# Optimization experiments

Measured on AMD Instinct MI355X. Metric: run time of the kernel, lower is better.

## Reference

```python
import jax, jax.numpy as jnp
import numpy as np

NUM_CLASSES = 10
LAMBDA_UNCERTAINTY = 0.5
IGNORE_INDEX = 10
B, H, W = 8, 512, 512


def setup_inputs() -> dict:
    key = jax.random.key(0)
    k1, k2 = jax.random.split(key)
    logits = jax.random.normal(k1, (B, NUM_CLASSES, H, W), dtype=jnp.float32)
    targets = jax.random.randint(k2, (B, H, W), 0, 11)  # includes ignore_index=10
    return {"logits": logits, "targets": targets}


def reference(logits, targets):
    C = NUM_CLASSES
    f32 = logits.dtype

    # entropy of the predicted distribution (torch adds 1e-8 inside log)
    probs = jax.nn.softmax(logits, axis=1)                      # [B,C,H,W]
    log_probs = jnp.log(probs + 1e-8)
    entropy = -jnp.sum(probs * log_probs, axis=1)               # [B,H,W]

    valid = targets != IGNORE_INDEX                             # [B,H,W] bool
    valid_f = valid.astype(f32)
    n_valid = jnp.sum(valid_f)                                  # scalar

    # single-pass scatter-mean replacing the per-class python loop
    t_clip = jnp.clip(targets, 0, C - 1)
    t_flat = t_clip.reshape(-1)
    v_flat = valid_f.reshape(-1)
    counts = jax.ops.segment_sum(v_flat, t_flat, num_segments=C)                    # n_c per class
    ent_sum = jax.ops.segment_sum(entropy.reshape(-1) * v_flat, t_flat, num_segments=C)

    has_samples = (counts > 0) & (n_valid > 0)
    w_base = jnp.where(has_samples, (n_valid - counts) / jnp.maximum(n_valid, 1.0), 0.0)
    entropy_mean = jnp.where(counts > 0, ent_sum / jnp.maximum(counts, 1.0), 0.0)
    w_combined = w_base * (1.0 + LAMBDA_UNCERTAINTY * entropy_mean)                 # [C]

    weight_map = w_combined[t_clip] * valid_f                   # [B,H,W]

    # per-pixel cross entropy, zeroed at ignore_index (torch F.cross_entropy semantics)
    log_sm = jax.nn.log_softmax(logits, axis=1)                 # [B,C,H,W]
    ce = -jnp.take_along_axis(log_sm, t_clip[:, None], axis=1)[:, 0]  # [B,H,W]
    ce = ce * valid_f

    return jnp.sum(ce * weight_map) / (n_valid + 1e-6)
```

## Files before the change

### kernel.cpp

```cpp
#include <hip/hip_runtime.h>

#define NCLS 10
#define IGN 10
#define HW_ (512 * 512)
#define BATCH 8
#define NPIX (BATCH * HW_)
#define THREADS 256
#define PIXPERTHREAD 4
#define NBLOCKS (NPIX / (THREADS * PIXPERTHREAD))
#define STAT_STRIDE 16
#define LAMBDA_UNC 0.5f

__global__ void awce_zero_stats(float* __restrict__ stats) {
    int i = threadIdx.x;
    if (i < 30 * STAT_STRIDE) stats[i] = 0.0f;
}

template <bool ATOMIC>
__global__ __launch_bounds__(THREADS) void awce_main(
    const float* __restrict__ logits,
    const int* __restrict__ targets,
    float* __restrict__ outbuf)
{
    const int gtid = blockIdx.x * THREADS + threadIdx.x;
    const int p0 = gtid * PIXPERTHREAD;
    const int b = p0 >> 18;
    const int hw = p0 & (HW_ - 1);
    const float* base = logits + (size_t)b * (NCLS * (size_t)HW_) + hw;

    float x[NCLS][4];
#pragma unroll
    for (int c = 0; c < NCLS; ++c) {
        float4 v = *reinterpret_cast<const float4*>(base + (size_t)c * HW_);
        x[c][0] = v.x; x[c][1] = v.y; x[c][2] = v.z; x[c][3] = v.w;
    }
    int4 t4 = *reinterpret_cast<const int4*>(targets + p0);
    int t[4] = {t4.x, t4.y, t4.z, t4.w};

    float cnt[NCLS], es[NCLS], cs[NCLS];
#pragma unroll
    for (int c = 0; c < NCLS; ++c) { cnt[c] = 0.f; es[c] = 0.f; cs[c] = 0.f; }

#pragma unroll
    for (int j = 0; j < PIXPERTHREAD; ++j) {
        const int tj = t[j];
        const bool valid = (tj != IGN);
        const int tc = valid ? tj : (NCLS - 1);

        float m = x[0][j];
#pragma unroll
        for (int c = 1; c < NCLS; ++c) m = fmaxf(m, x[c][j]);

        float s = 0.f, dot = 0.f, xt = 0.f;
#pragma unroll
        for (int c = 0; c < NCLS; ++c) {
            const float xc = x[c][j];
            const float e = __expf(xc - m);
            s += e;
            dot = fmaf(e, xc, dot);
            xt = (tc == c) ? xc : xt;
        }
        const float lse = m + __logf(s);
        const float ent = lse - dot / s;
        const float ce = lse - xt;

#pragma unroll
        for (int c = 0; c < NCLS; ++c) {
            const float match = (valid && (tc == c)) ? 1.f : 0.f;
            cnt[c] += match;
            es[c] = fmaf(match, ent, es[c]);
            cs[c] = fmaf(match, ce, cs[c]);
        }
    }

#pragma unroll
    for (int c = 0; c < NCLS; ++c) {
#pragma unroll
        for (int o = 32; o >= 1; o >>= 1) {
            cnt[c] += __shfl_xor(cnt[c], o);
            es[c]  += __shfl_xor(es[c],  o);
            cs[c]  += __shfl_xor(cs[c],  o);
        }
    }

    __shared__ float red[THREADS / 64][30];
    const int wave = threadIdx.x >> 6;
    const int lane = threadIdx.x & 63;
    if (lane == 0) {
#pragma unroll
        for (int c = 0; c < NCLS; ++c) {
            red[wave][c]      = cnt[c];
            red[wave][10 + c] = es[c];
            red[wave][20 + c] = cs[c];
        }
    }
    __syncthreads();
    const int sidx = threadIdx.x;
    if (sidx < 30) {
        float v = red[0][sidx] + red[1][sidx] + red[2][sidx] + red[3][sidx];
        if (ATOMIC) {
            atomicAdd(&outbuf[sidx * STAT_STRIDE], v);
        } else {
            outbuf[sidx * NBLOCKS + blockIdx.x] = v;
        }
    }
}

__global__ __launch_bounds__(512) void awce_final_partials(
    const float* __restrict__ partials, float* __restrict__ out)
{
    __shared__ float sred[32];
    const int wave = threadIdx.x >> 6;
    const int lane = threadIdx.x & 63;
#pragma unroll
    for (int k = 0; k < 4; ++k) {
        const int c = wave + k * 8;
        if (c < 30) {
            const float* col = partials + (size_t)c * NBLOCKS;
            float s = 0.f;
#pragma unroll
            for (int i = 0; i < NBLOCKS / 64; ++i) s += col[lane + 64 * i];
#pragma unroll
            for (int o = 32; o >= 1; o >>= 1) s += __shfl_xor(s, o);
            if (lane == 0) sred[c] = s;
        }
    }
    __syncthreads();
    if (threadIdx.x == 0) {
        float cnt[NCLS], es[NCLS], cs[NCLS];
        float nv = 0.f;
#pragma unroll
        for (int c = 0; c < NCLS; ++c) {
            cnt[c] = sred[c];
            es[c]  = sred[10 + c];
            cs[c]  = sred[20 + c];
            nv += cnt[c];
        }
        float loss = 0.f;
#pragma unroll
        for (int c = 0; c < NCLS; ++c) {
            float wb = 0.f;
            if (cnt[c] > 0.f && nv > 0.f) wb = (nv - cnt[c]) / fmaxf(nv, 1.f);
            const float em = (cnt[c] > 0.f) ? es[c] / fmaxf(cnt[c], 1.f) : 0.f;
            const float wc = wb * (1.f + LAMBDA_UNC * em);
            loss = fmaf(cs[c], wc, loss);
        }
        out[0] = loss / (nv + 1e-6f);
    }
}

__global__ void awce_final_atomic(const float* __restrict__ stats, float* __restrict__ out) {
    if (threadIdx.x == 0) {
        float cnt[NCLS], es[NCLS], cs[NCLS];
        float nv = 0.f;
#pragma unroll
        for (int c = 0; c < NCLS; ++c) {
            cnt[c] = stats[c * STAT_STRIDE];
            es[c]  = stats[(10 + c) * STAT_STRIDE];
            cs[c]  = stats[(20 + c) * STAT_STRIDE];
            nv += cnt[c];
        }
        float loss = 0.f;
#pragma unroll
        for (int c = 0; c < NCLS; ++c) {
            float wb = 0.f;
            if (cnt[c] > 0.f && nv > 0.f) wb = (nv - cnt[c]) / fmaxf(nv, 1.f);
            const float em = (cnt[c] > 0.f) ? es[c] / fmaxf(cnt[c], 1.f) : 0.f;
            const float wc = wb * (1.f + LAMBDA_UNC * em);
            loss = fmaf(cs[c], wc, loss);
        }
        out[0] = loss / (nv + 1e-6f);
    }
}

extern "C" void kernel_launch(void* const* d_in, const int* in_sizes, int n_in,
                              void* d_out, int out_size, void* d_ws, size_t ws_size,
                              hipStream_t stream) {
    const float* logits = (const float*)d_in[0];
    const int* targets = (const int*)d_in[1];
    float* out = (float*)d_out;
    float* ws = (float*)d_ws;

    const size_t need = (size_t)30 * NBLOCKS * sizeof(float);
    if (ws_size >= need) {
        awce_main<false><<<NBLOCKS, THREADS, 0, stream>>>(logits, targets, ws);
        awce_final_partials<<<1, 512, 0, stream>>>(ws, out);
    } else {
        awce_zero_stats<<<1, 512, 0, stream>>>(ws);
        awce_main<true><<<NBLOCKS, THREADS, 0, stream>>>(logits, targets, ws);
        awce_final_atomic<<<1, 64, 0, stream>>>(ws, out);
    }
}
```

Before: 32.56 us.

## Process four chunks per thread with double-buffered register prefetch

Each block now covers four chunks of pixels instead of one, which cuts the block count by four. The loads for the next chunk are issued into a second register buffer before the current chunk is processed, so memory latency overlaps with the softmax arithmetic. This also shrinks the per-block partials and the cost of the shuffle reductions. The trade-off is higher register pressure from two 40-float buffers, which may reduce occupancy, and fewer blocks to spread across the CUs.

```diff
diff --git a/kernel.cpp b/kernel.cpp
--- a/kernel.cpp
+++ b/kernel.cpp
@@ -7,7 +7,8 @@
 #define NPIX (BATCH * HW_)
 #define THREADS 256
 #define PIXPERTHREAD 4
-#define NBLOCKS (NPIX / (THREADS * PIXPERTHREAD))
+#define CHUNKS 4
+#define NBLOCKS (NPIX / (THREADS * PIXPERTHREAD * CHUNKS))
 #define STAT_STRIDE 16
 #define LAMBDA_UNC 0.5f
 
@@ -22,55 +23,75 @@
     const int* __restrict__ targets,
     float* __restrict__ outbuf)
 {
-    const int gtid = blockIdx.x * THREADS + threadIdx.x;
-    const int p0 = gtid * PIXPERTHREAD;
-    const int b = p0 >> 18;
-    const int hw = p0 & (HW_ - 1);
-    const float* base = logits + (size_t)b * (NCLS * (size_t)HW_) + hw;
-
-    float x[NCLS][4];
-#pragma unroll
-    for (int c = 0; c < NCLS; ++c) {
-        float4 v = *reinterpret_cast<const float4*>(base + (size_t)c * HW_);
-        x[c][0] = v.x; x[c][1] = v.y; x[c][2] = v.z; x[c][3] = v.w;
-    }
-    int4 t4 = *reinterpret_cast<const int4*>(targets + p0);
-    int t[4] = {t4.x, t4.y, t4.z, t4.w};
+    const int tid = threadIdx.x;
 
     float cnt[NCLS], es[NCLS], cs[NCLS];
 #pragma unroll
     for (int c = 0; c < NCLS; ++c) { cnt[c] = 0.f; es[c] = 0.f; cs[c] = 0.f; }
 
-#pragma unroll
-    for (int j = 0; j < PIXPERTHREAD; ++j) {
-        const int tj = t[j];
-        const bool valid = (tj != IGN);
-        const int tc = valid ? tj : (NCLS - 1);
-
-        float m = x[0][j];
-#pragma unroll
-        for (int c = 1; c < NCLS; ++c) m = fmaxf(m, x[c][j]);
-
-        float s = 0.f, dot = 0.f, xt = 0.f;
-#pragma unroll
-        for (int c = 0; c < NCLS; ++c) {
-            const float xc = x[c][j];
-            const float e = __expf(xc - m);
-            s += e;
-            dot = fmaf(e, xc, dot);
-            xt = (tc == c) ? xc : xt;
-        }
-        const float lse = m + __logf(s);
-        const float ent = lse - dot / s;
-        const float ce = lse - xt;
-
-#pragma unroll
-        for (int c = 0; c < NCLS; ++c) {
-            const float match = (valid && (tc == c)) ? 1.f : 0.f;
-            cnt[c] += match;
-            es[c] = fmaf(match, ent, es[c]);
-            cs[c] = fmaf(match, ce, cs[c]);
-        }
+    float xb_[2][NCLS][4];
+    int tb_[2][4];
+
+    auto chunk_p0 = [&](int k) {
+        return ((blockIdx.x * CHUNKS + k) * THREADS + tid) * PIXPERTHREAD;
+    };
+
+#define LOAD_CHUNK(k, slot)                                                        \
+    {                                                                              \
+        const int p0 = chunk_p0(k);                                                \
+        const int b = p0 >> 18;                                                    \
+        const int hw = p0 & (HW_ - 1);                                             \
+        const float* base = logits + (size_t)b * (NCLS * (size_t)HW_) + hw;        \
+        _Pragma("unroll")                                                          \
+        for (int c = 0; c < NCLS; ++c) {                                           \
+            float4 v = *reinterpret_cast<const float4*>(base + (size_t)c * HW_);   \
+            xb_[slot][c][0] = v.x; xb_[slot][c][1] = v.y;                          \
+            xb_[slot][c][2] = v.z; xb_[slot][c][3] = v.w;                          \
+        }                                                                          \
+        int4 t4 = *reinterpret_cast<const int4*>(targets + p0);                    \
+        tb_[slot][0] = t4.x; tb_[slot][1] = t4.y;                                  \
+        tb_[slot][2] = t4.z; tb_[slot][3] = t4.w;                                  \
+    }
+
+#define PROC_CHUNK(slot)                                                           \
+    {                                                                              \
+        _Pragma("unroll")                                                          \
+        for (int j = 0; j < PIXPERTHREAD; ++j) {                                   \
+            const int tj = tb_[slot][j];                                           \
+            const bool valid = (tj != IGN);                                        \
+            const int tc = valid ? tj : (NCLS - 1);                                \
+            float m = xb_[slot][0][j];                                             \
+            _Pragma("unroll")                                                      \
+            for (int c = 1; c < NCLS; ++c) m = fmaxf(m, xb_[slot][c][j]);          \
+            float s = 0.f, dot = 0.f, xt = 0.f;                                    \
+            _Pragma("unroll")                                                      \
+            for (int c = 0; c < NCLS; ++c) {                                       \
+                const float xc = xb_[slot][c][j];                                  \
+                const float e = __expf(xc - m);                                    \
+                s += e;                                                            \
+                dot = fmaf(e, xc, dot);                                            \
+                xt = (tc == c) ? xc : xt;                                          \
+            }                                                                      \
+            const float lse = m + __logf(s);                                       \
+            const float ent = lse - dot / s;                                       \
+            const float ce = lse - xt;                                             \
+            _Pragma("unroll")                                                      \
+            for (int c = 0; c < NCLS; ++c) {                                       \
+                const float match = (valid && (tc == c)) ? 1.f : 0.f;              \
+                cnt[c] += match;                                                   \
+                es[c] = fmaf(match, ent, es[c]);                                   \
+                cs[c] = fmaf(match, ce, cs[c]);                                    \
+            }                                                                      \
+        }                                                                          \
+    }
+
+    LOAD_CHUNK(0, 0)
+#pragma unroll
+    for (int k = 0; k < CHUNKS; ++k) {
+        if (k + 1 < CHUNKS) {
+            if ((k + 1) & 1) LOAD_CHUNK(k + 1, 1) else LOAD_CHUNK(k + 1, 0)
+        }
+        if (k & 1) PROC_CHUNK(1) else PROC_CHUNK(0)
     }
 
 #pragma unroll
@@ -84,8 +105,8 @@
     }
 
     __shared__ float red[THREADS / 64][30];
-    const int wave = threadIdx.x >> 6;
-    const int lane = threadIdx.x & 63;
+    const int wave = tid >> 6;
+    const int lane = tid & 63;
     if (lane == 0) {
 #pragma unroll
         for (int c = 0; c < NCLS; ++c) {
@@ -95,15 +116,16 @@
         }
     }
     __syncthreads();
-    const int sidx = threadIdx.x;
-    if (sidx < 30) {
-        float v = red[0][sidx] + red[1][sidx] + red[2][sidx] + red[3][sidx];
+    if (tid < 30) {
+        float v = red[0][tid] + red[1][tid] + red[2][tid] + red[3][tid];
         if (ATOMIC) {
-            atomicAdd(&outbuf[sidx * STAT_STRIDE], v);
+            atomicAdd(&outbuf[tid * STAT_STRIDE], v);
         } else {
-            outbuf[sidx * NBLOCKS + blockIdx.x] = v;
-        }
-    }
+            outbuf[tid * NBLOCKS + blockIdx.x] = v;
+        }
+    }
+#undef LOAD_CHUNK
+#undef PROC_CHUNK
 }
 
 __global__ __launch_bounds__(512) void awce_final_partials(
```

New measurement: 27.71 us. 1.17x faster.

## Stage logits into LDS with double-buffered async loads and per-thread LDS histograms

Applied to the files above, without the earlier changes.

The main kernel now gives each block 4 chunks of 512 pixels and stages logits and targets into shared memory using global_load_lds, double-buffered so the next chunk's load overlaps the current chunk's compute. Per-class statistics accumulate in a per-thread padded LDS histogram indexed by target, replacing the 30-value per-thread register accumulators and their shuffle reductions. The exp and log use native exp2/log and rcp intrinsics. The cost is more LDS per block, lower occupancy and a syncthreads per chunk. The block count drops, so the final partial-reduction kernel (which still assumes NBLOCKS divisible by 64) reads fewer partials.

```diff
diff --git a/kernel.cpp b/kernel.cpp
--- a/kernel.cpp
+++ b/kernel.cpp
@@ -6,10 +6,24 @@
 #define BATCH 8
 #define NPIX (BATCH * HW_)
 #define THREADS 256
-#define PIXPERTHREAD 4
-#define NBLOCKS (NPIX / (THREADS * PIXPERTHREAD))
+#define PPT 2
+#define CHUNK_PX (THREADS * PPT)
+#define CHUNKS 4
+#define BLOCK_PX (CHUNK_PX * CHUNKS)
+#define NBLOCKS (NPIX / BLOCK_PX)
 #define STAT_STRIDE 16
 #define LAMBDA_UNC 0.5f
+#define LOG2E 1.4426950408889634f
+#define LN2 0.6931471805599453f
+
+#define RSTRIDE 33
+#define HISTSZ (THREADS * RSTRIDE)
+
+typedef const __attribute__((address_space(1))) void GV;
+typedef __attribute__((address_space(3))) void LV;
+__device__ __forceinline__ void gload_lds16(const void* g, void* l) {
+    __builtin_amdgcn_global_load_lds((GV*)g, (LV*)l, 16, 0, 0);
+}
 
 __global__ void awce_zero_stats(float* __restrict__ stats) {
     int i = threadIdx.x;
@@ -22,86 +36,100 @@
     const int* __restrict__ targets,
     float* __restrict__ outbuf)
 {
-    const int gtid = blockIdx.x * THREADS + threadIdx.x;
-    const int p0 = gtid * PIXPERTHREAD;
-    const int b = p0 >> 18;
-    const int hw = p0 & (HW_ - 1);
-    const float* base = logits + (size_t)b * (NCLS * (size_t)HW_) + hw;
-
-    float x[NCLS][4];
-#pragma unroll
-    for (int c = 0; c < NCLS; ++c) {
-        float4 v = *reinterpret_cast<const float4*>(base + (size_t)c * HW_);
-        x[c][0] = v.x; x[c][1] = v.y; x[c][2] = v.z; x[c][3] = v.w;
-    }
-    int4 t4 = *reinterpret_cast<const int4*>(targets + p0);
-    int t[4] = {t4.x, t4.y, t4.z, t4.w};
-
-    float cnt[NCLS], es[NCLS], cs[NCLS];
-#pragma unroll
-    for (int c = 0; c < NCLS; ++c) { cnt[c] = 0.f; es[c] = 0.f; cs[c] = 0.f; }
-
-#pragma unroll
-    for (int j = 0; j < PIXPERTHREAD; ++j) {
-        const int tj = t[j];
-        const bool valid = (tj != IGN);
-        const int tc = valid ? tj : (NCLS - 1);
-
-        float m = x[0][j];
-#pragma unroll
-        for (int c = 1; c < NCLS; ++c) m = fmaxf(m, x[c][j]);
-
-        float s = 0.f, dot = 0.f, xt = 0.f;
-#pragma unroll
-        for (int c = 0; c < NCLS; ++c) {
-            const float xc = x[c][j];
-            const float e = __expf(xc - m);
-            s += e;
-            dot = fmaf(e, xc, dot);
-            xt = (tc == c) ? xc : xt;
-        }
-        const float lse = m + __logf(s);
-        const float ent = lse - dot / s;
-        const float ce = lse - xt;
-
-#pragma unroll
-        for (int c = 0; c < NCLS; ++c) {
-            const float match = (valid && (tc == c)) ? 1.f : 0.f;
-            cnt[c] += match;
-            es[c] = fmaf(match, ent, es[c]);
-            cs[c] = fmaf(match, ce, cs[c]);
-        }
-    }
-
-#pragma unroll
-    for (int c = 0; c < NCLS; ++c) {
-#pragma unroll
-        for (int o = 32; o >= 1; o >>= 1) {
-            cnt[c] += __shfl_xor(cnt[c], o);
-            es[c]  += __shfl_xor(es[c],  o);
-            cs[c]  += __shfl_xor(cs[c],  o);
-        }
-    }
-
-    __shared__ float red[THREADS / 64][30];
-    const int wave = threadIdx.x >> 6;
-    const int lane = threadIdx.x & 63;
-    if (lane == 0) {
-#pragma unroll
-        for (int c = 0; c < NCLS; ++c) {
-            red[wave][c]      = cnt[c];
-            red[wave][10 + c] = es[c];
-            red[wave][20 + c] = cs[c];
-        }
-    }
+    const int tid = threadIdx.x;
+    const int wave = tid >> 6;
+    const int lane = tid & 63;
+
+    __shared__ float stage[2][11][CHUNK_PX];
+    __shared__ float hist[HISTSZ];
+    __shared__ float red[4][32];
+
+    const int g0 = blockIdx.x * BLOCK_PX;
+    const int b = g0 >> 18;
+    const int hw0 = g0 & (HW_ - 1);
+    const float* lbase = logits + (size_t)b * (NCLS * (size_t)HW_);
+
+    auto stage_chunk = [&](int k, int s) {
+#pragma unroll
+        for (int i = wave; i < 22; i += 4) {
+            const int c = i >> 1;
+            const int h = i & 1;
+            const int pxo = h * 256 + (lane << 2);
+            const void* gsrc;
+            if (c < 10)
+                gsrc = (const void*)(lbase + (size_t)c * HW_ + hw0 + k * CHUNK_PX + pxo);
+            else
+                gsrc = (const void*)(targets + g0 + k * CHUNK_PX + pxo);
+            gload_lds16(gsrc, (void*)&stage[s][c][h * 256]);
+        }
+    };
+
+    stage_chunk(0, 0);
+#pragma unroll
+    for (int i = 0; i < RSTRIDE; ++i) hist[tid + i * THREADS] = 0.0f;
     __syncthreads();
-    const int sidx = threadIdx.x;
-    if (sidx < 30) {
-        float v = red[0][sidx] + red[1][sidx] + red[2][sidx] + red[3][sidx];
+
+    float* hreg = &hist[tid * RSTRIDE];
+
+#pragma unroll
+    for (int k = 0; k < CHUNKS; ++k) {
+        const int s = k & 1;
+        float x[NCLS][PPT];
+#pragma unroll
+        for (int c = 0; c < NCLS; ++c) {
+            float2 v = *reinterpret_cast<float2*>(&stage[s][c][tid * PPT]);
+            x[c][0] = v.x; x[c][1] = v.y;
+        }
+        int2 tt = *reinterpret_cast<int2*>(&stage[s][10][tid * PPT]);
+        int t2[PPT] = {tt.x, tt.y};
+        __builtin_amdgcn_sched_barrier(0);
+        if (k + 1 < CHUNKS) stage_chunk(k + 1, s ^ 1);
+#pragma unroll
+        for (int j = 0; j < PPT; ++j) {
+            const int tj = t2[j];
+            const int tc = (tj != IGN) ? tj : NCLS;
+            float m = x[0][j];
+#pragma unroll
+            for (int c = 1; c < NCLS; ++c) m = fmaxf(m, x[c][j]);
+            const float nm2 = -m * LOG2E;
+            float sum = 0.f, dot = 0.f, xt = 0.f;
+#pragma unroll
+            for (int c = 0; c < NCLS; ++c) {
+                const float xc = x[c][j];
+                const float e = __builtin_amdgcn_exp2f(fmaf(xc, LOG2E, nm2));
+                sum += e;
+                dot = fmaf(e, xc, dot);
+                xt = (tc == c) ? xc : xt;
+            }
+            const float lse = fmaf(__builtin_amdgcn_logf(sum), LN2, m);
+            const float rs = __builtin_amdgcn_rcpf(sum);
+            const float ent = fmaf(-dot, rs, lse);
+            const float ce = lse - xt;
+            float* p = hreg + 3 * tc;
+            p[0] += 1.0f;
+            p[1] += ent;
+            p[2] += ce;
+        }
+        __syncthreads();
+    }
+
+    if (lane < 30) {
+        const int f = (lane >= 20) ? 2 : ((lane >= 10) ? 1 : 0);
+        const int c = lane - f * 10;
+        const int off = 3 * c + f;
+        float v = 0.f;
+#pragma unroll
+        for (int r = 0; r < 64; ++r) v += hist[(wave * 64 + r) * RSTRIDE + off];
+        red[wave][lane] = v;
+    }
+    __syncthreads();
+
+    if (tid < 30) {
+        float v = red[0][tid] + red[1][tid] + red[2][tid] + red[3][tid];
         if (ATOMIC) {
-            atomicAdd(&outbuf[sidx * STAT_STRIDE], v);
+            atomicAdd(&outbuf[tid * STAT_STRIDE], v);
         } else {
-            outbuf[sidx * NBLOCKS + blockIdx.x] = v;
+            outbuf[tid * NBLOCKS + blockIdx.x] = v;
         }
     }
 }
```

New measurement: 26.84 us. 17.6% less time.
